# Performance work log

Hardware: AMD Instinct MI355X
Metric: run time of the kernel (lower is better)

Reference implementation:

```python
import jax, jax.numpy as jnp
import numpy as np

N, C, H = 256, 128, 4
D = C // H


def setup_inputs() -> dict:
    key = jax.random.key(0)
    ks = jax.random.split(key, 7)
    pair_rep = jax.random.normal(ks[0], (N, N, C), dtype=jnp.float32)
    distance_matrix = jax.random.normal(ks[1], (N, N), dtype=jnp.float32)
    Wqkv = jax.random.normal(ks[2], (C, 3 * C), dtype=jnp.float32) * (1.0 / np.sqrt(C))
    bqkv = jax.random.normal(ks[3], (3 * C,), dtype=jnp.float32) * 0.02
    Wout = jax.random.normal(ks[4], (C, C), dtype=jnp.float32) * (1.0 / np.sqrt(C))
    bout = jax.random.normal(ks[5], (C,), dtype=jnp.float32) * 0.02
    dscale = jnp.ones((1,), dtype=jnp.float32)
    mask = jax.random.randint(ks[6], (N, N), 0, 2).astype(jnp.bool_)
    return {"pair_rep": pair_rep, "distance_matrix": distance_matrix, "Wqkv": Wqkv,
            "bqkv": bqkv, "Wout": Wout, "bout": bout, "dscale": dscale, "mask": mask}


def reference(pair_rep, distance_matrix, Wqkv, bqkv, Wout, bout, dscale, mask):
    n = pair_rep.shape[0]
    qkv = pair_rep @ Wqkv + bqkv                      # [n,n,3c]
    q, k, v = jnp.split(qkv, 3, axis=-1)
    q = q.reshape(n, n, H, D)
    k = k.reshape(n, n, H, D)
    v = v.reshape(n, n, H, D)
    # scores[h,i,j,k] = q[i,j,h,:] . k[i,k,h,:] / sqrt(D)
    scores = jnp.einsum('ijhd,ikhd->hijk', q, k) / np.sqrt(D)
    bias = (dscale[0] * distance_matrix)[None, None, :, :]   # [1,1,n,n]
    scores = scores + bias
    scores = jnp.where(mask[None, None, :, :], -jnp.inf, scores)
    attn = jax.nn.softmax(scores, axis=-1)            # [H,n,n,n]
    out = jnp.einsum('hijk,ikhd->ijhd', attn, v).reshape(n, n, C)
    return out @ Wout + bout
```

## Files before the change

kernel.cpp:

```cpp
#include <hip/hip_runtime.h>
#include <hip/hip_bf16.h>
#include <math.h>

#define NN 256
#define CC 128
#define HH 4
#define DD 32

typedef uint4 u128;
typedef __bf16 bf16x8 __attribute__((ext_vector_type(8)));
typedef float f32x4 __attribute__((ext_vector_type(4)));

#define LOG2E 1.4426950408889634f
#define QSC (0.17677669529663687f * LOG2E)

__global__ __launch_bounds__(256) void prep_kernel(
    const float* __restrict__ dm, const int* __restrict__ mask,
    const float* __restrict__ dscale,
    const float* __restrict__ Wqkv, const float* __restrict__ Wout,
    const float* __restrict__ pair,
    float* __restrict__ biasM,
    __hip_bfloat16* __restrict__ Wt_qkv, __hip_bfloat16* __restrict__ Wt_out,
    __hip_bfloat16* __restrict__ Abf)
{
    const int b = blockIdx.x, t = threadIdx.x;
    if (b < 256) {
        int idx = b * 256 + t;
        biasM[idx] = mask[idx] ? -INFINITY : dscale[0] * dm[idx] * LOG2E;
    } else if (b < 448) {
        int idx = (b - 256) * 256 + t;
        int n = idx >> 7, k = idx & 127;
        Wt_qkv[idx] = __float2bfloat16(Wqkv[(size_t)k * 384 + n]);
    } else if (b < 512) {
        int idx = (b - 448) * 256 + t;
        int n = idx >> 7, k = idx & 127;
        Wt_out[idx] = __float2bfloat16(Wout[(size_t)k * CC + n]);
    } else {
        size_t e = (size_t)(b - 512) * 2048 + (size_t)t * 8;
        float4 v0 = *(const float4*)(pair + e);
        float4 v1 = *(const float4*)(pair + e + 4);
        __hip_bfloat162 a01 = __float22bfloat162_rn(float2{v0.x, v0.y});
        __hip_bfloat162 a23 = __float22bfloat162_rn(float2{v0.z, v0.w});
        __hip_bfloat162 a45 = __float22bfloat162_rn(float2{v1.x, v1.y});
        __hip_bfloat162 a67 = __float22bfloat162_rn(float2{v1.z, v1.w});
        u128 pk;
        pk.x = *(unsigned int*)&a01;
        pk.y = *(unsigned int*)&a23;
        pk.z = *(unsigned int*)&a45;
        pk.w = *(unsigned int*)&a67;
        *(u128*)&Abf[e] = pk;
    }
}

__global__ __launch_bounds__(512, 4) void qkv_mfma_kernel(
    const __hip_bfloat16* __restrict__ A,
    const __hip_bfloat16* __restrict__ Bt,
    const float* __restrict__ bias,
    __hip_bfloat16* __restrict__ out)
{
    __shared__ __align__(16) __hip_bfloat16 As[128][136];
    __shared__ __align__(16) __hip_bfloat16 Bs[96][136];
    const int t = threadIdx.x;
    const int m0 = blockIdx.x * 128;
    const int n0 = blockIdx.y * 96;

    #pragma unroll
    for (int it = 0; it < 4; ++it) {
        int idx = it * 512 + t;
        int r = idx >> 4, c8 = (idx & 15) * 8;
        *(u128*)&As[r][c8] = *(const u128*)(A + (size_t)(m0 + r) * CC + c8);
    }
    #pragma unroll
    for (int it = 0; it < 3; ++it) {
        int idx = it * 512 + t;
        int n = idx >> 4, c8 = (idx & 15) * 8;
        *(u128*)&Bs[n][c8] = *(const u128*)(Bt + (size_t)(n0 + n) * CC + c8);
    }
    __syncthreads();

    const int w = t >> 6, lane = t & 63;
    const int n16 = lane & 15, quad = lane >> 4;
    const int mw = (w & 3) * 32, nw = (w >> 2) * 48;

    bf16x8 pf[2][4];
    #pragma unroll
    for (int mt = 0; mt < 2; ++mt)
        #pragma unroll
        for (int ks = 0; ks < 4; ++ks)
            pf[mt][ks] = *(const bf16x8*)&As[mw + mt * 16 + n16][ks * 32 + quad * 8];

    f32x4 acc[2][3];
    #pragma unroll
    for (int mt = 0; mt < 2; ++mt)
        #pragma unroll
        for (int nt = 0; nt < 3; ++nt) acc[mt][nt] = (f32x4){0.f, 0.f, 0.f, 0.f};

    #pragma unroll
    for (int nt = 0; nt < 3; ++nt) {
        bf16x8 wf[4];
        #pragma unroll
        for (int ks = 0; ks < 4; ++ks)
            wf[ks] = *(const bf16x8*)&Bs[nw + nt * 16 + n16][ks * 32 + quad * 8];
        #pragma unroll
        for (int ks = 0; ks < 4; ++ks)
            #pragma unroll
            for (int mt = 0; mt < 2; ++mt)
                acc[mt][nt] = __builtin_amdgcn_mfma_f32_16x16x32_bf16(wf[ks], pf[mt][ks], acc[mt][nt], 0, 0, 0);
    }

    #pragma unroll
    for (int nt = 0; nt < 3; ++nt) {
        int nbase = n0 + nw + nt * 16 + quad * 4;
        float4 b4 = *(const float4*)(bias + nbase);
        float sc = (nbase < CC) ? QSC : 1.0f;
        #pragma unroll
        for (int mt = 0; mt < 2; ++mt) {
            int m = m0 + mw + mt * 16 + n16;
            __hip_bfloat162 h01 = __float22bfloat162_rn(float2{(acc[mt][nt][0] + b4.x) * sc, (acc[mt][nt][1] + b4.y) * sc});
            __hip_bfloat162 h23 = __float22bfloat162_rn(float2{(acc[mt][nt][2] + b4.z) * sc, (acc[mt][nt][3] + b4.w) * sc});
            uint2 pk;
            pk.x = *(unsigned int*)&h01;
            pk.y = *(unsigned int*)&h23;
            *(uint2*)&out[(size_t)m * 384 + nbase] = pk;
        }
    }
}

__global__ __launch_bounds__(512, 8) void attn_mfma_kernel(
    const __hip_bfloat16* __restrict__ qkv,
    const float* __restrict__ biasM,
    __hip_bfloat16* __restrict__ attn_out)
{
    __shared__ __align__(16) __hip_bfloat16 Ks[NN][40];
    __shared__ __align__(16) __hip_bfloat16 VTs[DD][264];

    const int bi = blockIdx.x;
    const int i = bi >> 2, h = bi & 3;
    const int t = threadIdx.x;

    {
        const int r = t >> 1, half = t & 1;
        const __hip_bfloat16* base = qkv + (size_t)(i * NN + r) * 384 + h * DD;
        const u128* ksrc = (const u128*)(base + CC) + half * 2;
        u128* kdst = (u128*)&Ks[r][0] + half * 2;
        kdst[0] = ksrc[0];
        kdst[1] = ksrc[1];
        const u128* vsrc = (const u128*)(base + 2 * CC) + half * 2;
        u128 vr[2];
        vr[0] = vsrc[0];
        vr[1] = vsrc[1];
        const __hip_bfloat16* vh = (const __hip_bfloat16*)vr;
        const int pr = (r & ~0x1F) | ((r & 0xC) << 1) | ((r & 0x10) >> 2) | (r & 0x3);
        #pragma unroll
        for (int dd = 0; dd < 16; ++dd) VTs[half * 16 + dd][pr] = vh[dd];
    }
    __syncthreads();

    const int w = t >> 6, lane = t & 63;
    const int n16 = lane & 15, quad = lane >> 4;

    #pragma unroll
    for (int jt = 0; jt < 2; ++jt) {
        const int j0 = w * 32 + jt * 16;
        const int j = j0 + n16;

        bf16x8 qa = *(const bf16x8*)(qkv + (size_t)(i * NN + j) * 384 + h * DD + quad * 8);
        const float4* brow = (const float4*)(biasM + (size_t)j * NN);

        f32x4 sm = {0.f, 0.f, 0.f, 0.f};
        f32x4 o0 = {0.f, 0.f, 0.f, 0.f}, o1 = {0.f, 0.f, 0.f, 0.f};

        #pragma unroll 2
        for (int c = 0; c < 8; ++c) {
            float4 b0 = brow[c * 8 + quad];
            float4 b1 = brow[c * 8 + 4 + quad];
            bf16x8 kb0 = *(const bf16x8*)&Ks[c * 32 + n16][quad * 8];
            bf16x8 kb1 = *(const bf16x8*)&Ks[c * 32 + 16 + n16][quad * 8];
            f32x4 s0 = __builtin_amdgcn_mfma_f32_16x16x32_bf16(
                kb0, qa, (f32x4){b0.x, b0.y, b0.z, b0.w}, 0, 0, 0);
            f32x4 s1 = __builtin_amdgcn_mfma_f32_16x16x32_bf16(
                kb1, qa, (f32x4){b1.x, b1.y, b1.z, b1.w}, 0, 0, 0);

            float p0 = __builtin_amdgcn_exp2f(s0[0]);
            float p1 = __builtin_amdgcn_exp2f(s0[1]);
            float p2 = __builtin_amdgcn_exp2f(s0[2]);
            float p3 = __builtin_amdgcn_exp2f(s0[3]);
            float p4 = __builtin_amdgcn_exp2f(s1[0]);
            float p5 = __builtin_amdgcn_exp2f(s1[1]);
            float p6 = __builtin_amdgcn_exp2f(s1[2]);
            float p7 = __builtin_amdgcn_exp2f(s1[3]);
            sm[0] += p0 + p4;
            sm[1] += p1 + p5;
            sm[2] += p2 + p6;
            sm[3] += p3 + p7;

            __hip_bfloat162 q01 = __float22bfloat162_rn(float2{p0, p1});
            __hip_bfloat162 q23 = __float22bfloat162_rn(float2{p2, p3});
            __hip_bfloat162 q45 = __float22bfloat162_rn(float2{p4, p5});
            __hip_bfloat162 q67 = __float22bfloat162_rn(float2{p6, p7});
            u128 pk;
            pk.x = *(unsigned int*)&q01;
            pk.y = *(unsigned int*)&q23;
            pk.z = *(unsigned int*)&q45;
            pk.w = *(unsigned int*)&q67;
            bf16x8 pa = *(bf16x8*)&pk;

            bf16x8 vb0 = *(const bf16x8*)&VTs[n16][c * 32 + quad * 8];
            bf16x8 vb1 = *(const bf16x8*)&VTs[16 + n16][c * 32 + quad * 8];
            o0 = __builtin_amdgcn_mfma_f32_16x16x32_bf16(vb0, pa, o0, 0, 0, 0);
            o1 = __builtin_amdgcn_mfma_f32_16x16x32_bf16(vb1, pa, o1, 0, 0, 0);
        }

        float sum = (sm[0] + sm[1]) + (sm[2] + sm[3]);
        sum += __shfl_xor(sum, 16);
        sum += __shfl_xor(sum, 32);
        float inv = 1.0f / sum;

        __hip_bfloat16* obase = attn_out + (size_t)(i * NN + j) * CC + h * DD + quad * 4;
        {
            __hip_bfloat162 h01 = __float22bfloat162_rn(float2{o0[0] * inv, o0[1] * inv});
            __hip_bfloat162 h23 = __float22bfloat162_rn(float2{o0[2] * inv, o0[3] * inv});
            uint2 pk;
            pk.x = *(unsigned int*)&h01;
            pk.y = *(unsigned int*)&h23;
            *(uint2*)(obase) = pk;
        }
        {
            __hip_bfloat162 h01 = __float22bfloat162_rn(float2{o1[0] * inv, o1[1] * inv});
            __hip_bfloat162 h23 = __float22bfloat162_rn(float2{o1[2] * inv, o1[3] * inv});
            uint2 pk;
            pk.x = *(unsigned int*)&h01;
            pk.y = *(unsigned int*)&h23;
            *(uint2*)(obase + 16) = pk;
        }
    }
}

__global__ __launch_bounds__(512, 4) void out_mfma_kernel(
    const __hip_bfloat16* __restrict__ A,
    const __hip_bfloat16* __restrict__ Bt,
    const float* __restrict__ bias,
    float* __restrict__ out)
{
    __shared__ __align__(16) __hip_bfloat16 As[128][136];
    __shared__ __align__(16) __hip_bfloat16 Bs[128][136];
    const int t = threadIdx.x;
    const int m0 = blockIdx.x * 128;

    #pragma unroll
    for (int it = 0; it < 4; ++it) {
        int idx = it * 512 + t;
        int r = idx >> 4, c8 = (idx & 15) * 8;
        *(u128*)&As[r][c8] = *(const u128*)(A + (size_t)(m0 + r) * CC + c8);
    }
    #pragma unroll
    for (int it = 0; it < 4; ++it) {
        int idx = it * 512 + t;
        int n = idx >> 4, c8 = (idx & 15) * 8;
        *(u128*)&Bs[n][c8] = *(const u128*)(Bt + (size_t)n * CC + c8);
    }
    __syncthreads();

    const int w = t >> 6, lane = t & 63;
    const int n16 = lane & 15, quad = lane >> 4;
    const int mw = (w & 3) * 32, nw = (w >> 2) * 64;

    bf16x8 pf[2][4];
    #pragma unroll
    for (int mt = 0; mt < 2; ++mt)
        #pragma unroll
        for (int ks = 0; ks < 4; ++ks)
            pf[mt][ks] = *(const bf16x8*)&As[mw + mt * 16 + n16][ks * 32 + quad * 8];

    f32x4 acc[2][4];
    #pragma unroll
    for (int mt = 0; mt < 2; ++mt)
        #pragma unroll
        for (int nt = 0; nt < 4; ++nt) acc[mt][nt] = (f32x4){0.f, 0.f, 0.f, 0.f};

    #pragma unroll
    for (int nt = 0; nt < 4; ++nt) {
        bf16x8 wf[4];
        #pragma unroll
        for (int ks = 0; ks < 4; ++ks)
            wf[ks] = *(const bf16x8*)&Bs[nw + nt * 16 + n16][ks * 32 + quad * 8];
        #pragma unroll
        for (int ks = 0; ks < 4; ++ks)
            #pragma unroll
            for (int mt = 0; mt < 2; ++mt)
                acc[mt][nt] = __builtin_amdgcn_mfma_f32_16x16x32_bf16(wf[ks], pf[mt][ks], acc[mt][nt], 0, 0, 0);
    }

    #pragma unroll
    for (int nt = 0; nt < 4; ++nt) {
        int nbase = nw + nt * 16 + quad * 4;
        float4 b4 = *(const float4*)(bias + nbase);
        #pragma unroll
        for (int mt = 0; mt < 2; ++mt) {
            int m = m0 + mw + mt * 16 + n16;
            float4 ov;
            ov.x = acc[mt][nt][0] + b4.x;
            ov.y = acc[mt][nt][1] + b4.y;
            ov.z = acc[mt][nt][2] + b4.z;
            ov.w = acc[mt][nt][3] + b4.w;
            *(float4*)&out[(size_t)m * CC + nbase] = ov;
        }
    }
}

extern "C" void kernel_launch(void* const* d_in, const int* in_sizes, int n_in,
                              void* d_out, int out_size, void* d_ws, size_t ws_size,
                              hipStream_t stream) {
    const float* pair_rep = (const float*)d_in[0];
    const float* dm       = (const float*)d_in[1];
    const float* Wqkv     = (const float*)d_in[2];
    const float* bqkv     = (const float*)d_in[3];
    const float* Wout     = (const float*)d_in[4];
    const float* bout     = (const float*)d_in[5];
    const float* dscale   = (const float*)d_in[6];
    const int*   mask     = (const int*)d_in[7];
    float* out = (float*)d_out;

    char* p = (char*)d_ws;
    float* biasM = (float*)p;                 p += (size_t)NN * NN * 4;
    __hip_bfloat16* Wt_qkv = (__hip_bfloat16*)p;  p += (size_t)384 * CC * 2;
    __hip_bfloat16* Wt_out = (__hip_bfloat16*)p;  p += (size_t)CC * CC * 2;
    __hip_bfloat16* qkv  = (__hip_bfloat16*)p;    p += (size_t)65536 * 384 * 2;
    __hip_bfloat16* attn = (__hip_bfloat16*)p;
    __hip_bfloat16* Abf  = attn;

    prep_kernel<<<dim3(4608), dim3(256), 0, stream>>>(dm, mask, dscale, Wqkv, Wout, pair_rep, biasM, Wt_qkv, Wt_out, Abf);
    qkv_mfma_kernel<<<dim3(512, 4), dim3(512), 0, stream>>>(Abf, Wt_qkv, bqkv, qkv);
    attn_mfma_kernel<<<dim3(1024), dim3(512), 0, stream>>>(qkv, biasM, attn);
    out_mfma_kernel<<<dim3(512), dim3(512), 0, stream>>>(attn, Wt_out, bout, out);
}
```

Baseline: 167.2 us.

## Fuse fp32-to-bf16 input conversion into QKV GEMM and pre-swizzle bias layout

Drops the separate pass that converted pair_rep to a bf16 workspace copy. The QKV GEMM now reads fp32 pair_rep directly and converts it while filling LDS, which removes one full write and re-read of the activation buffer. The bias/mask matrix is also written in an MFMA-fragment-ordered layout, so each lane in the attention kernel loads a contiguous float4 per lane instead of strided row reads. In exchange, each of the 4 column blocks of the QKV GEMM re-reads the fp32 input, which is twice the bytes of the bf16 copy.

Measured after the change: 160.8 us. 1.04x faster.

```diff
diff --git a/kernel.cpp b/kernel.cpp
--- a/kernel.cpp
+++ b/kernel.cpp
@@ -18,42 +18,30 @@
     const float* __restrict__ dm, const int* __restrict__ mask,
     const float* __restrict__ dscale,
     const float* __restrict__ Wqkv, const float* __restrict__ Wout,
-    const float* __restrict__ pair,
-    float* __restrict__ biasM,
-    __hip_bfloat16* __restrict__ Wt_qkv, __hip_bfloat16* __restrict__ Wt_out,
-    __hip_bfloat16* __restrict__ Abf)
+    float* __restrict__ bias2,
+    __hip_bfloat16* __restrict__ Wt_qkv, __hip_bfloat16* __restrict__ Wt_out)
 {
     const int b = blockIdx.x, t = threadIdx.x;
     if (b < 256) {
-        int idx = b * 256 + t;
-        biasM[idx] = mask[idx] ? -INFINITY : dscale[0] * dm[idx] * LOG2E;
+        const int j = b, k = t;
+        int idx = j * 256 + k;
+        float v = mask[idx] ? -INFINITY : dscale[0] * dm[idx] * LOG2E;
+        int c = k >> 5, bb = (k >> 4) & 1, quad = (k >> 2) & 3, r = k & 3;
+        int dst = ((((c * 2 + bb) * 16 + (j >> 4)) * 64) + quad * 16 + (j & 15)) * 4 + r;
+        bias2[dst] = v;
     } else if (b < 448) {
         int idx = (b - 256) * 256 + t;
         int n = idx >> 7, k = idx & 127;
         Wt_qkv[idx] = __float2bfloat16(Wqkv[(size_t)k * 384 + n]);
-    } else if (b < 512) {
+    } else {
         int idx = (b - 448) * 256 + t;
         int n = idx >> 7, k = idx & 127;
         Wt_out[idx] = __float2bfloat16(Wout[(size_t)k * CC + n]);
-    } else {
-        size_t e = (size_t)(b - 512) * 2048 + (size_t)t * 8;
-        float4 v0 = *(const float4*)(pair + e);
-        float4 v1 = *(const float4*)(pair + e + 4);
-        __hip_bfloat162 a01 = __float22bfloat162_rn(float2{v0.x, v0.y});
-        __hip_bfloat162 a23 = __float22bfloat162_rn(float2{v0.z, v0.w});
-        __hip_bfloat162 a45 = __float22bfloat162_rn(float2{v1.x, v1.y});
-        __hip_bfloat162 a67 = __float22bfloat162_rn(float2{v1.z, v1.w});
-        u128 pk;
-        pk.x = *(unsigned int*)&a01;
-        pk.y = *(unsigned int*)&a23;
-        pk.z = *(unsigned int*)&a45;
-        pk.w = *(unsigned int*)&a67;
-        *(u128*)&Abf[e] = pk;
     }
 }
 
 __global__ __launch_bounds__(512, 4) void qkv_mfma_kernel(
-    const __hip_bfloat16* __restrict__ A,
+    const float* __restrict__ A,
     const __hip_bfloat16* __restrict__ Bt,
     const float* __restrict__ bias,
     __hip_bfloat16* __restrict__ out)
@@ -65,10 +53,16 @@
     const int n0 = blockIdx.y * 96;
 
     #pragma unroll
-    for (int it = 0; it < 4; ++it) {
+    for (int it = 0; it < 8; ++it) {
         int idx = it * 512 + t;
-        int r = idx >> 4, c8 = (idx & 15) * 8;
-        *(u128*)&As[r][c8] = *(const u128*)(A + (size_t)(m0 + r) * CC + c8);
+        int r = idx >> 5, c4 = (idx & 31) * 4;
+        float4 v = *(const float4*)(A + (size_t)(m0 + r) * CC + c4);
+        __hip_bfloat162 a01 = __float22bfloat162_rn(float2{v.x, v.y});
+        __hip_bfloat162 a23 = __float22bfloat162_rn(float2{v.z, v.w});
+        uint2 pk;
+        pk.x = *(unsigned int*)&a01;
+        pk.y = *(unsigned int*)&a23;
+        *(uint2*)&As[r][c4] = pk;
     }
     #pragma unroll
     for (int it = 0; it < 3; ++it) {
@@ -128,7 +122,7 @@
 
 __global__ __launch_bounds__(512, 8) void attn_mfma_kernel(
     const __hip_bfloat16* __restrict__ qkv,
-    const float* __restrict__ biasM,
+    const float* __restrict__ bias2,
     __hip_bfloat16* __restrict__ attn_out)
 {
     __shared__ __align__(16) __hip_bfloat16 Ks[NN][40];
@@ -163,17 +157,18 @@
     for (int jt = 0; jt < 2; ++jt) {
         const int j0 = w * 32 + jt * 16;
         const int j = j0 + n16;
+        const int jblk = w * 2 + jt;
 
         bf16x8 qa = *(const bf16x8*)(qkv + (size_t)(i * NN + j) * 384 + h * DD + quad * 8);
-        const float4* brow = (const float4*)(biasM + (size_t)j * NN);
+        const float4* bb = (const float4*)bias2;
 
         f32x4 sm = {0.f, 0.f, 0.f, 0.f};
         f32x4 o0 = {0.f, 0.f, 0.f, 0.f}, o1 = {0.f, 0.f, 0.f, 0.f};
 
         #pragma unroll 2
         for (int c = 0; c < 8; ++c) {
-            float4 b0 = brow[c * 8 + quad];
-            float4 b1 = brow[c * 8 + 4 + quad];
+            float4 b0 = bb[((c * 2 + 0) * 16 + jblk) * 64 + lane];
+            float4 b1 = bb[((c * 2 + 1) * 16 + jblk) * 64 + lane];
             bf16x8 kb0 = *(const bf16x8*)&Ks[c * 32 + n16][quad * 8];
             bf16x8 kb1 = *(const bf16x8*)&Ks[c * 32 + 16 + n16][quad * 8];
             f32x4 s0 = __builtin_amdgcn_mfma_f32_16x16x32_bf16(
@@ -322,15 +317,14 @@
     float* out = (float*)d_out;
 
     char* p = (char*)d_ws;
-    float* biasM = (float*)p;                 p += (size_t)NN * NN * 4;
+    float* bias2 = (float*)p;                 p += (size_t)NN * NN * 4;
     __hip_bfloat16* Wt_qkv = (__hip_bfloat16*)p;  p += (size_t)384 * CC * 2;
     __hip_bfloat16* Wt_out = (__hip_bfloat16*)p;  p += (size_t)CC * CC * 2;
     __hip_bfloat16* qkv  = (__hip_bfloat16*)p;    p += (size_t)65536 * 384 * 2;
     __hip_bfloat16* attn = (__hip_bfloat16*)p;
-    __hip_bfloat16* Abf  = attn;
-
-    prep_kernel<<<dim3(4608), dim3(256), 0, stream>>>(dm, mask, dscale, Wqkv, Wout, pair_rep, biasM, Wt_qkv, Wt_out, Abf);
-    qkv_mfma_kernel<<<dim3(512, 4), dim3(512), 0, stream>>>(Abf, Wt_qkv, bqkv, qkv);
-    attn_mfma_kernel<<<dim3(1024), dim3(512), 0, stream>>>(qkv, biasM, attn);
+
+    prep_kernel<<<dim3(512), dim3(256), 0, stream>>>(dm, mask, dscale, Wqkv, Wout, bias2, Wt_qkv, Wt_out);
+    qkv_mfma_kernel<<<dim3(512, 4), dim3(512), 0, stream>>>(pair_rep, Wt_qkv, bqkv, qkv);
+    attn_mfma_kernel<<<dim3(1024), dim3(512), 0, stream>>>(qkv, bias2, attn);
     out_mfma_kernel<<<dim3(512), dim3(512), 0, stream>>>(attn, Wt_out, bout, out);
 }
```
